# Performance work log

Hardware: AMD Instinct MI355X
Metric: run time of the kernel (lower is better)

Reference implementation:

```python
import jax, jax.numpy as jnp
import numpy as np

HEADS = 8
MAX_BUCKETS = 128
DIM = 128          # = 2 * d_h
TEMPERATURE = 0.7
SINKHORN_ITERS = 8
EPS = 1e-6


def setup_inputs() -> dict:
    key = jax.random.key(0)
    k1, k2, k3, k4, k5 = jax.random.split(key, 5)
    B, T, DH = 4, 16384, 64
    q = jax.random.normal(k1, (B * HEADS, T, DH), dtype=jnp.float32)
    k = jax.random.normal(k2, (B * HEADS, T, DH), dtype=jnp.float32)
    linear = jax.random.normal(k3, (1, HEADS, DIM, MAX_BUCKETS), dtype=jnp.float32)
    segment_ids = jnp.sort(
        jax.random.randint(k4, (B, T), 0, MAX_BUCKETS), axis=-1
    ).astype(jnp.int32)
    gumbel_u = jax.random.uniform(k5, (B * HEADS, MAX_BUCKETS, MAX_BUCKETS), dtype=jnp.float32)
    return {"q": q, "k": k, "linear": linear, "segment_ids": segment_ids, "gumbel_u": gumbel_u}


def _forward(q, k, linear, segment_ids, gumbel_u):
    bh, t, dh = q.shape           # (b*heads, t, d_h)
    b = segment_ids.shape[0]
    heads = bh // b
    # replicate per-sample bucket assignment across heads (sample-major layout)
    ids = jnp.repeat(segment_ids, heads, axis=0)          # (bh, t)
    seg_sum = jax.vmap(lambda x, s: jax.ops.segment_sum(x, s, num_segments=MAX_BUCKETS))
    sq = seg_sum(q, ids)                                  # (bh, nb, d_h)
    sk = seg_sum(k, ids)                                  # (bh, nb, d_h)
    x = jnp.concatenate([sq, sk], axis=-1)                # (bh, nb, 2*d_h)
    # expand linear over batch and merge head dim: (bh, dim, max_buckets)
    W = jnp.broadcast_to(linear, (b,) + linear.shape[1:]).reshape(bh, DIM, MAX_BUCKETS)
    R = jax.nn.relu(jnp.einsum("bnd,bdm->bnm", x, W))     # (bh, nb, mb)
    # gumbel sinkhorn
    r = jnp.log(R + EPS)
    g = -jnp.log(-jnp.log(gumbel_u + EPS) + EPS)
    r = (r + g) / TEMPERATURE
    for _ in range(SINKHORN_ITERS):
        r = r - jax.nn.logsumexp(r, axis=2, keepdims=True)
        r = r - jax.nn.logsumexp(r, axis=1, keepdims=True)
    return jnp.exp(r)


def reference(q, k, linear, segment_ids, gumbel_u):
    return _forward(q, k, linear, segment_ids, gumbel_u)
```

## Files before the change

kernel.cpp:

```cpp
#include <hip/hip_runtime.h>
#include <hip/hip_bf16.h>

constexpr int HEADS = 8;
constexpr int B = 4;
constexpr int BH = B * HEADS;
constexpr int T = 16384;
constexpr int DH = 64;
constexpr int NB = 128;
constexpr int DIM = 128;
constexpr float EPS = 1e-6f;
constexpr float INV_TEMP = 1.0f / 0.7f;

constexpr int CHUNK = 1024;

__global__ __launch_bounds__(256) void k_segsum(
    const float* __restrict__ q, const float* __restrict__ k,
    const int* __restrict__ seg, float* __restrict__ x) {
  const int bh = blockIdx.y;
  const int b = bh >> 3;
  const int t0 = blockIdx.x * CHUNK;
  const int tid = threadIdx.x;

  __shared__ float sums[NB][2 * DH];
  __shared__ int ids[CHUNK];

  for (int i = tid; i < CHUNK; i += 256) ids[i] = seg[(size_t)b * T + t0 + i];
  __syncthreads();

  const int bmin = ids[0];
  const int bmax = ids[CHUNK - 1];
  const int nzero = (bmax - bmin + 1) * 128;
  float* sflat = &sums[bmin][0];
  for (int i = tid; i < nzero; i += 256) sflat[i] = 0.f;
  __syncthreads();

  const int slot = tid & 31;
  const int grp = tid >> 5;
  const bool isq = slot < 16;
  const int f4 = slot & 15;
  const float4* src =
      (const float4*)((isq ? q : k) + (size_t)bh * T * DH) + (size_t)t0 * 16 + f4;
  const int loff = (isq ? 0 : DH) + f4 * 4;

  float4 acc = make_float4(0.f, 0.f, 0.f, 0.f);
  int cur = -1;
  for (int t = grp; t < CHUNK; t += 8) {
    const int bk = ids[t];
    const float4 v = src[(size_t)t * 16];
    if (bk != cur) {
      if (cur >= 0) {
        atomicAdd(&sums[cur][loff + 0], acc.x);
        atomicAdd(&sums[cur][loff + 1], acc.y);
        atomicAdd(&sums[cur][loff + 2], acc.z);
        atomicAdd(&sums[cur][loff + 3], acc.w);
      }
      acc = v;
      cur = bk;
    } else {
      acc.x += v.x; acc.y += v.y; acc.z += v.z; acc.w += v.w;
    }
  }
  if (cur >= 0) {
    atomicAdd(&sums[cur][loff + 0], acc.x);
    atomicAdd(&sums[cur][loff + 1], acc.y);
    atomicAdd(&sums[cur][loff + 2], acc.z);
    atomicAdd(&sums[cur][loff + 3], acc.w);
  }
  __syncthreads();

  float* xp = x + (size_t)bh * NB * 128 + (size_t)bmin * 128;
  for (int i = tid; i < nzero; i += 256) {
    const float v = sflat[i];
    if (v != 0.f) atomicAdd(&xp[i], v);
  }
}

__global__ __launch_bounds__(256) void k_matmul(
    const float* __restrict__ x, const float* __restrict__ linear,
    const float* __restrict__ gumbel, float* __restrict__ r0) {
  const int bh = blockIdx.y;
  const int n0 = blockIdx.x * 16;
  const int h = bh & 7;
  const int tid = threadIdx.x;

  __shared__ float xs[16][DIM];

  const float4* xp = (const float4*)(x + ((size_t)bh * NB + n0) * DIM);
  for (int i = tid; i < 16 * 32; i += 256) {
    const float4 v = xp[i];
    const int n = i >> 5, d4 = i & 31;
    xs[n][d4 * 4 + 0] = v.x;
    xs[n][d4 * 4 + 1] = v.y;
    xs[n][d4 * 4 + 2] = v.z;
    xs[n][d4 * 4 + 3] = v.w;
  }
  __syncthreads();

  const int mt = tid & 31;
  const int rp = tid >> 5;
  const int ra = rp * 2;

  float4 a0 = make_float4(0.f, 0.f, 0.f, 0.f);
  float4 a1 = make_float4(0.f, 0.f, 0.f, 0.f);
  const float4* Wp = (const float4*)(linear + (size_t)h * DIM * NB);
  for (int d4 = 0; d4 < 32; d4++) {
    const float4 xv0 = *(const float4*)&xs[ra][d4 * 4];
    const float4 xv1 = *(const float4*)&xs[ra + 1][d4 * 4];
    const float4 w0 = Wp[(d4 * 4 + 0) * 32 + mt];
    const float4 w1 = Wp[(d4 * 4 + 1) * 32 + mt];
    const float4 w2 = Wp[(d4 * 4 + 2) * 32 + mt];
    const float4 w3 = Wp[(d4 * 4 + 3) * 32 + mt];
    a0.x += xv0.x * w0.x + xv0.y * w1.x + xv0.z * w2.x + xv0.w * w3.x;
    a0.y += xv0.x * w0.y + xv0.y * w1.y + xv0.z * w2.y + xv0.w * w3.y;
    a0.z += xv0.x * w0.z + xv0.y * w1.z + xv0.z * w2.z + xv0.w * w3.z;
    a0.w += xv0.x * w0.w + xv0.y * w1.w + xv0.z * w2.w + xv0.w * w3.w;
    a1.x += xv1.x * w0.x + xv1.y * w1.x + xv1.z * w2.x + xv1.w * w3.x;
    a1.y += xv1.x * w0.y + xv1.y * w1.y + xv1.z * w2.y + xv1.w * w3.y;
    a1.z += xv1.x * w0.z + xv1.y * w1.z + xv1.z * w2.z + xv1.w * w3.z;
    a1.w += xv1.x * w0.w + xv1.y * w1.w + xv1.z * w2.w + xv1.w * w3.w;
  }

  const float4* gp = (const float4*)(gumbel + ((size_t)bh * NB + n0) * NB);
  float4* op = (float4*)(r0 + ((size_t)bh * NB + n0) * NB);

  auto xform = [](float a, float u) {
    const float R = fmaxf(a, 0.f);
    const float g = -logf(-logf(u + EPS) + EPS);
    return (logf(R + EPS) + g) * INV_TEMP;
  };
  {
    const float4 u = gp[(size_t)ra * 32 + mt];
    float4 o;
    o.x = xform(a0.x, u.x); o.y = xform(a0.y, u.y);
    o.z = xform(a0.z, u.z); o.w = xform(a0.w, u.w);
    op[(size_t)ra * 32 + mt] = o;
  }
  {
    const float4 u = gp[(size_t)(ra + 1) * 32 + mt];
    float4 o;
    o.x = xform(a1.x, u.x); o.y = xform(a1.y, u.y);
    o.z = xform(a1.z, u.z); o.w = xform(a1.w, u.w);
    op[(size_t)(ra + 1) * 32 + mt] = o;
  }
}

__global__ __launch_bounds__(512) void k_sinkhorn(
    const float* __restrict__ r0, float* __restrict__ out) {
  const int bh = blockIdx.x;
  const int tid = threadIdx.x;

  __shared__ float r[NB][NB + 1];
  __shared__ float lse_r[NB];
  __shared__ float lse_c[NB];

  const float4* rp = (const float4*)(r0 + (size_t)bh * NB * NB);
  for (int i = tid; i < NB * 32; i += 512) {
    const float4 v = rp[i];
    const int n = i >> 5, m4 = i & 31;
    r[n][m4 * 4 + 0] = v.x;
    r[n][m4 * 4 + 1] = v.y;
    r[n][m4 * 4 + 2] = v.z;
    r[n][m4 * 4 + 3] = v.w;
  }
  __syncthreads();

  const int row = tid >> 2;
  const int qp = tid & 3;

  for (int it = 0; it < 8; it++) {
    float mx = -1e30f;
#pragma unroll
    for (int j = 0; j < 32; j++) {
      const int m = qp * 32 + ((j + qp * 8) & 31);
      mx = fmaxf(mx, r[row][m]);
    }
    mx = fmaxf(mx, __shfl_xor(mx, 1));
    mx = fmaxf(mx, __shfl_xor(mx, 2));
    float s = 0.f;
#pragma unroll
    for (int j = 0; j < 32; j++) {
      const int m = qp * 32 + ((j + qp * 8) & 31);
      s += expf(r[row][m] - mx);
    }
    s += __shfl_xor(s, 1);
    s += __shfl_xor(s, 2);
    if (qp == 0) lse_r[row] = mx + logf(s);
    __syncthreads();

    const int col = row;
    float cmx = -1e30f;
#pragma unroll
    for (int j = 0; j < 32; j++) {
      const int n = qp * 32 + ((j + qp * 8) & 31);
      cmx = fmaxf(cmx, r[n][col] - lse_r[n]);
    }
    cmx = fmaxf(cmx, __shfl_xor(cmx, 1));
    cmx = fmaxf(cmx, __shfl_xor(cmx, 2));
    float cs = 0.f;
#pragma unroll
    for (int j = 0; j < 32; j++) {
      const int n = qp * 32 + ((j + qp * 8) & 31);
      cs += expf(r[n][col] - lse_r[n] - cmx);
    }
    cs += __shfl_xor(cs, 1);
    cs += __shfl_xor(cs, 2);
    if (qp == 0) lse_c[col] = cmx + logf(cs);
    __syncthreads();

    const float lr = lse_r[row];
#pragma unroll
    for (int j = 0; j < 32; j++) {
      const int m = qp * 32 + ((j + qp * 8) & 31);
      r[row][m] = r[row][m] - lr - lse_c[m];
    }
    __syncthreads();
  }

  float* op = out + (size_t)bh * NB * NB;
  for (int i = tid; i < NB * NB; i += 512) {
    const int n = i >> 7, m = i & 127;
    op[i] = expf(r[n][m]);
  }
}

extern "C" void kernel_launch(void* const* d_in, const int* in_sizes, int n_in,
                              void* d_out, int out_size, void* d_ws, size_t ws_size,
                              hipStream_t stream) {
  const float* q = (const float*)d_in[0];
  const float* k = (const float*)d_in[1];
  const float* linear = (const float*)d_in[2];
  const int* seg = (const int*)d_in[3];
  const float* gum = (const float*)d_in[4];
  float* out = (float*)d_out;

  float* x = (float*)d_ws;
  float* r0 = out;

  hipMemsetAsync(x, 0, (size_t)BH * NB * DIM * sizeof(float), stream);

  dim3 g1(T / CHUNK, BH);
  k_segsum<<<g1, 256, 0, stream>>>(q, k, seg, x);

  dim3 g2(8, BH);
  k_matmul<<<g2, 256, 0, stream>>>(x, linear, gum, r0);

  k_sinkhorn<<<BH, 512, 0, stream>>>(r0, out);
}
```

Measured before the change: 364.1 us.

## Stream segsum straight to global atomics, register-resident sinkhorn, fast math

The segment-sum kernel drops its shared-memory bucket table and instead gives each warp a contiguous 128-token run, unrolled by 8 with loads issued before the id checks. Run boundaries are flushed directly to global memory with atomics. The sinkhorn kernel keeps each thread's 32 row elements in registers and uses shared memory only as a transpose image for the column logsumexp, which drops a barrier per iteration. Fast __expf/__logf intrinsics replace expf/logf in the matmul and sinkhorn kernels, at some cost in accuracy. The global atomics may contend more, but the segment ids are sorted, so flushes are rare.

```diff
diff --git a/kernel.cpp b/kernel.cpp
--- a/kernel.cpp
+++ b/kernel.cpp
@@ -12,6 +12,7 @@
 constexpr float INV_TEMP = 1.0f / 0.7f;
 
 constexpr int CHUNK = 1024;
+constexpr int TPG = 128;
 
 __global__ __launch_bounds__(256) void k_segsum(
     const float* __restrict__ q, const float* __restrict__ k,
@@ -21,57 +22,58 @@
   const int t0 = blockIdx.x * CHUNK;
   const int tid = threadIdx.x;
 
-  __shared__ float sums[NB][2 * DH];
   __shared__ int ids[CHUNK];
-
   for (int i = tid; i < CHUNK; i += 256) ids[i] = seg[(size_t)b * T + t0 + i];
-  __syncthreads();
-
-  const int bmin = ids[0];
-  const int bmax = ids[CHUNK - 1];
-  const int nzero = (bmax - bmin + 1) * 128;
-  float* sflat = &sums[bmin][0];
-  for (int i = tid; i < nzero; i += 256) sflat[i] = 0.f;
   __syncthreads();
 
   const int slot = tid & 31;
   const int grp = tid >> 5;
   const bool isq = slot < 16;
   const int f4 = slot & 15;
-  const float4* src =
-      (const float4*)((isq ? q : k) + (size_t)bh * T * DH) + (size_t)t0 * 16 + f4;
-  const int loff = (isq ? 0 : DH) + f4 * 4;
+  const int base = grp * TPG;
+  const float4* src = (const float4*)((isq ? q : k) + (size_t)bh * T * DH) +
+                      (size_t)(t0 + base) * 16 + f4;
+  float* xb = x + (size_t)bh * NB * 128 + (isq ? 0 : DH) + f4 * 4;
 
   float4 acc = make_float4(0.f, 0.f, 0.f, 0.f);
-  int cur = -1;
-  for (int t = grp; t < CHUNK; t += 8) {
-    const int bk = ids[t];
-    const float4 v = src[(size_t)t * 16];
-    if (bk != cur) {
-      if (cur >= 0) {
-        atomicAdd(&sums[cur][loff + 0], acc.x);
-        atomicAdd(&sums[cur][loff + 1], acc.y);
-        atomicAdd(&sums[cur][loff + 2], acc.z);
-        atomicAdd(&sums[cur][loff + 3], acc.w);
+  int cur = ids[base];
+
+  for (int j = 0; j < TPG; j += 8) {
+    float4 v0 = src[(size_t)(j + 0) * 16];
+    float4 v1 = src[(size_t)(j + 1) * 16];
+    float4 v2 = src[(size_t)(j + 2) * 16];
+    float4 v3 = src[(size_t)(j + 3) * 16];
+    float4 v4 = src[(size_t)(j + 4) * 16];
+    float4 v5 = src[(size_t)(j + 5) * 16];
+    float4 v6 = src[(size_t)(j + 6) * 16];
+    float4 v7 = src[(size_t)(j + 7) * 16];
+    int i0 = ids[base + j + 0], i1 = ids[base + j + 1];
+    int i2 = ids[base + j + 2], i3 = ids[base + j + 3];
+    int i4 = ids[base + j + 4], i5 = ids[base + j + 5];
+    int i6 = ids[base + j + 6], i7 = ids[base + j + 7];
+
+    auto step = [&](int bk, const float4& v) {
+      if (bk != cur) {
+        float* p = xb + (size_t)cur * 128;
+        atomicAdd(p + 0, acc.x);
+        atomicAdd(p + 1, acc.y);
+        atomicAdd(p + 2, acc.z);
+        atomicAdd(p + 3, acc.w);
+        acc = v;
+        cur = bk;
+      } else {
+        acc.x += v.x; acc.y += v.y; acc.z += v.z; acc.w += v.w;
       }
-      acc = v;
-      cur = bk;
-    } else {
-      acc.x += v.x; acc.y += v.y; acc.z += v.z; acc.w += v.w;
-    }
-  }
-  if (cur >= 0) {
-    atomicAdd(&sums[cur][loff + 0], acc.x);
-    atomicAdd(&sums[cur][loff + 1], acc.y);
-    atomicAdd(&sums[cur][loff + 2], acc.z);
-    atomicAdd(&sums[cur][loff + 3], acc.w);
-  }
-  __syncthreads();
-
-  float* xp = x + (size_t)bh * NB * 128 + (size_t)bmin * 128;
-  for (int i = tid; i < nzero; i += 256) {
-    const float v = sflat[i];
-    if (v != 0.f) atomicAdd(&xp[i], v);
+    };
+    step(i0, v0); step(i1, v1); step(i2, v2); step(i3, v3);
+    step(i4, v4); step(i5, v5); step(i6, v6); step(i7, v7);
+  }
+  {
+    float* p = xb + (size_t)cur * 128;
+    atomicAdd(p + 0, acc.x);
+    atomicAdd(p + 1, acc.y);
+    atomicAdd(p + 2, acc.z);
+    atomicAdd(p + 3, acc.w);
   }
 }
 
@@ -125,8 +127,8 @@
 
   auto xform = [](float a, float u) {
     const float R = fmaxf(a, 0.f);
-    const float g = -logf(-logf(u + EPS) + EPS);
-    return (logf(R + EPS) + g) * INV_TEMP;
+    const float g = -__logf(-__logf(u + EPS) + EPS);
+    return (__logf(R + EPS) + g) * INV_TEMP;
   };
   {
     const float4 u = gp[(size_t)ra * 32 + mt];
@@ -149,77 +151,77 @@
   const int bh = blockIdx.x;
   const int tid = threadIdx.x;
 
-  __shared__ float r[NB][NB + 1];
-  __shared__ float lse_r[NB];
+  __shared__ float img[NB * (NB + 1)];
   __shared__ float lse_c[NB];
-
-  const float4* rp = (const float4*)(r0 + (size_t)bh * NB * NB);
-  for (int i = tid; i < NB * 32; i += 512) {
-    const float4 v = rp[i];
-    const int n = i >> 5, m4 = i & 31;
-    r[n][m4 * 4 + 0] = v.x;
-    r[n][m4 * 4 + 1] = v.y;
-    r[n][m4 * 4 + 2] = v.z;
-    r[n][m4 * 4 + 3] = v.w;
-  }
-  __syncthreads();
 
   const int row = tid >> 2;
   const int qp = tid & 3;
 
+  float rr[32];
+  {
+    const float4* rp =
+        (const float4*)(r0 + (size_t)bh * NB * NB + row * NB + qp * 32);
+#pragma unroll
+    for (int u = 0; u < 8; u++) {
+      const float4 v = rp[u];
+      rr[4 * u + 0] = v.x; rr[4 * u + 1] = v.y;
+      rr[4 * u + 2] = v.z; rr[4 * u + 3] = v.w;
+    }
+  }
+
   for (int it = 0; it < 8; it++) {
-    float mx = -1e30f;
-#pragma unroll
-    for (int j = 0; j < 32; j++) {
-      const int m = qp * 32 + ((j + qp * 8) & 31);
-      mx = fmaxf(mx, r[row][m]);
-    }
-    mx = fmaxf(mx, __shfl_xor(mx, 1));
-    mx = fmaxf(mx, __shfl_xor(mx, 2));
+    float m = rr[0];
+#pragma unroll
+    for (int j = 1; j < 32; j++) m = fmaxf(m, rr[j]);
+    m = fmaxf(m, __shfl_xor(m, 1));
+    m = fmaxf(m, __shfl_xor(m, 2));
     float s = 0.f;
 #pragma unroll
-    for (int j = 0; j < 32; j++) {
-      const int m = qp * 32 + ((j + qp * 8) & 31);
-      s += expf(r[row][m] - mx);
-    }
+    for (int j = 0; j < 32; j++) s += __expf(rr[j] - m);
     s += __shfl_xor(s, 1);
     s += __shfl_xor(s, 2);
-    if (qp == 0) lse_r[row] = mx + logf(s);
+    const float lse = m + __logf(s);
+#pragma unroll
+    for (int j = 0; j < 32; j++) rr[j] -= lse;
+
+#pragma unroll
+    for (int j = 0; j < 32; j++) img[row * (NB + 1) + qp * 32 + j] = rr[j];
     __syncthreads();
 
-    const int col = row;
-    float cmx = -1e30f;
+    float tmp[32];
 #pragma unroll
     for (int j = 0; j < 32; j++) {
       const int n = qp * 32 + ((j + qp * 8) & 31);
-      cmx = fmaxf(cmx, r[n][col] - lse_r[n]);
+      tmp[j] = img[n * (NB + 1) + row];
     }
-    cmx = fmaxf(cmx, __shfl_xor(cmx, 1));
-    cmx = fmaxf(cmx, __shfl_xor(cmx, 2));
+    float cm = tmp[0];
+#pragma unroll
+    for (int j = 1; j < 32; j++) cm = fmaxf(cm, tmp[j]);
+    cm = fmaxf(cm, __shfl_xor(cm, 1));
+    cm = fmaxf(cm, __shfl_xor(cm, 2));
     float cs = 0.f;
 #pragma unroll
-    for (int j = 0; j < 32; j++) {
-      const int n = qp * 32 + ((j + qp * 8) & 31);
-      cs += expf(r[n][col] - lse_r[n] - cmx);
-    }
+    for (int j = 0; j < 32; j++) cs += __expf(tmp[j] - cm);
     cs += __shfl_xor(cs, 1);
     cs += __shfl_xor(cs, 2);
-    if (qp == 0) lse_c[col] = cmx + logf(cs);
+    if (qp == 0) lse_c[row] = cm + __logf(cs);
     __syncthreads();
 
-    const float lr = lse_r[row];
-#pragma unroll
-    for (int j = 0; j < 32; j++) {
-      const int m = qp * 32 + ((j + qp * 8) & 31);
-      r[row][m] = r[row][m] - lr - lse_c[m];
+#pragma unroll
+    for (int j = 0; j < 32; j++) rr[j] -= lse_c[qp * 32 + j];
+  }
+
+  {
+    float4* op = (float4*)(out + (size_t)bh * NB * NB + row * NB + qp * 32);
+#pragma unroll
+    for (int u = 0; u < 8; u++) {
+      float4 v;
+      v.x = __expf(rr[4 * u + 0]);
+      v.y = __expf(rr[4 * u + 1]);
+      v.z = __expf(rr[4 * u + 2]);
+      v.w = __expf(rr[4 * u + 3]);
+      op[u] = v;
     }
-    __syncthreads();
-  }
-
-  float* op = out + (size_t)bh * NB * NB;
-  for (int i = tid; i < NB * NB; i += 512) {
-    const int n = i >> 7, m = i & 127;
-    op[i] = expf(r[n][m]);
   }
 }
 
```

After: 331.7 us. 8.9% less time.
